# Optimization experiments

Hardware: AMD Instinct MI355X
Metric: run time of the kernel (lower is better)

The kernel has to match this reference:

```python
import jax, jax.numpy as jnp
import numpy as np

P, N, NF = 4, 871, 512            # num_meta_paths, node_size (hardcoded 871 in source), node_feature_size
XDIM = 116 * 116                   # x_proj input dim, hardcoded Linear(116*116, nf)
BETA, LAMBDA_WL, GAMMA = 0.1, 0.1, 0.1


def _xavier(k, shape):
    fan_in, fan_out = shape[0], shape[-1]
    bound = np.sqrt(6.0 / (fan_in + fan_out))
    return jax.random.uniform(k, shape, jnp.float32, -bound, bound)


def setup_inputs() -> dict:
    key = jax.random.key(0)
    ks = jax.random.split(key, 12)
    return {
        "z_stack": jax.random.normal(ks[0], (P, N, NF), jnp.float32),
        "x_orig": jax.random.normal(ks[1], (1, 116, 116), jnp.float32),
        "W": _xavier(ks[2], (N, 1)),
        "b": jax.random.uniform(ks[3], (N, 1), jnp.float32),
        "q": _xavier(ks[4], (N, NF)),
        "xp_w": _xavier(ks[5], (XDIM, NF)),
        "xp_b": jnp.zeros((NF,), jnp.float32),
        "w1": _xavier(ks[6], (2 * NF, 512)), "b1": jnp.zeros((512,), jnp.float32),
        "w2": _xavier(ks[7], (512, 256)), "b2": jnp.zeros((256,), jnp.float32),
        "w3": _xavier(ks[8], (256, 1)), "b3": jnp.zeros((1,), jnp.float32),
        "perm": jax.random.permutation(ks[9], N).astype(jnp.int32),
    }


def _mi_mlp(t, w1, b1, w2, b2, w3, b3):
    h = jax.nn.relu(t @ w1 + b1)
    h = jax.nn.relu(h @ w2 + b2)
    return h @ w3 + b3  # [N, 1]


def reference(z_stack, x_orig, W, b, q, xp_w, xp_b, w1, b1, w2, b2, w3, b3, perm):
    # --- vectorized form of the per-node loop:
    # score_p = mean_i( tanh(W_i * z[p,i,:] + b_i) . q_i )
    zt = jnp.tanh(W[None] * z_stack + b[None])            # [P,N,NF]
    scores = jnp.mean(jnp.sum(zt * q[None], axis=-1), axis=-1)  # [P]
    proportions = scores / jnp.sum(scores)
    attn = jax.nn.softmax(proportions)                    # [P] (no isomorphic pairs -> no overwrite)
    # layer_out_p = attn_p * z_p + z_p ; emb = sum_p layer_out_p
    emb = jnp.einsum('p,pnf->nf', 1.0 + attn, z_stack)    # [N,NF]
    # --- estimate_MI(x_orig, emb, mi_estimator_xz)
    x = jnp.broadcast_to(x_orig.reshape(1, -1), (N, XDIM))
    xh = x @ xp_w + xp_b                                  # [N,NF]
    t0 = jnp.concatenate([xh, emb], axis=1)               # [N,2NF]
    t1 = jnp.concatenate([xh, emb[perm]], axis=1)
    mi_lb = jnp.mean(_mi_mlp(t0, w1, b1, w2, b2, w3, b3)) - jnp.log(
        jnp.mean(jnp.exp(_mi_mlp(t1, w1, b1, w2, b2, w3, b3))) + 1e-8)
    I_XZ = jnp.clip(mi_lb, 0.0)
    # y_labels=None -> I_ZY = 0 ; empty isomorphic_pairs -> wl_loss = 0
    total_loss = I_XZ - BETA * 0.0 + LAMBDA_WL * 0.0 + GAMMA * jnp.sum(attn)
    return emb, total_loss
```

## Files before the change

kernel.cpp:

```cpp
#include <hip/hip_runtime.h>
#include <hip/hip_bf16.h>
#include <math.h>

#define NMETA  4
#define NNODE  871
#define NFEAT  512
#define XDIM   (116*116)
#define ZPLANE (NNODE*NFEAT)
#define Z4     (ZPLANE/4)
#define NCHUNK 55
#define MPAD   896
#define MT     56

#define WS_SCORES 0
#define WS_C1     528
#define WS_E1     1040
#define WS_XHP    WS_E1
#define WS_EMBB   (WS_E1 + MPAD*NFEAT)
#define WS_H2     WS_EMBB
#define WS_V      (WS_EMBB + MPAD*NFEAT/2)
#define WS_W1P    690040
#define WS_W2P    (WS_W1P + 512*512/2)

typedef short v8s __attribute__((ext_vector_type(8)));
typedef float v4f __attribute__((ext_vector_type(4)));

static __device__ __forceinline__ short f2bf(float f) {
  __hip_bfloat16 h = __float2bfloat16(f);
  return *reinterpret_cast<short*>(&h);
}

static __device__ __forceinline__ void compute_coef(const float* __restrict__ ws, float* coef) {
  float s[NMETA], sum = 0.f;
#pragma unroll
  for (int p = 0; p < NMETA; ++p) { s[p] = ws[WS_SCORES + p] / (float)NNODE; sum += s[p]; }
  float prop[NMETA], m = -1e30f;
#pragma unroll
  for (int p = 0; p < NMETA; ++p) { prop[p] = s[p] / sum; m = fmaxf(m, prop[p]); }
  float e[NMETA], es = 0.f;
#pragma unroll
  for (int p = 0; p < NMETA; ++p) { e[p] = expf(prop[p] - m); es += e[p]; }
#pragma unroll
  for (int p = 0; p < NMETA; ++p) coef[p] = 1.f + e[p] / es;
}

__global__ void k_init(float* __restrict__ ws) {
  int t = blockIdx.x * 256 + threadIdx.x;
  if (t < 1040) ws[t] = 0.f;
  else if (t < 1040 + (MPAD - NNODE) * NFEAT / 2)
    ws[WS_EMBB + NNODE * NFEAT / 2 + (t - 1040)] = 0.f;
}

__global__ void k_scores(const float* __restrict__ z, const float* __restrict__ W,
                         const float* __restrict__ b, const float* __restrict__ q,
                         float* __restrict__ ws) {
  const int p = blockIdx.x / NCHUNK;
  const int chunk = blockIdx.x % NCHUNK;
  const int i0 = chunk * 16;
  const int i1 = min(i0 + 16, NNODE);
  const int f4 = threadIdx.x & 127;
  const int ip = threadIdx.x >> 7;
  float local = 0.f;
  for (int i = i0 + ip; i < i1; i += 2) {
    const float wi = W[i];
    const float bi = b[i];
    const float4 zr = ((const float4*)(z + ((size_t)p * NNODE + i) * NFEAT))[f4];
    const float4 qr = ((const float4*)(q + (size_t)i * NFEAT))[f4];
    local += tanhf(wi * zr.x + bi) * qr.x + tanhf(wi * zr.y + bi) * qr.y
           + tanhf(wi * zr.z + bi) * qr.z + tanhf(wi * zr.w + bi) * qr.w;
  }
  __shared__ float red[256];
  red[threadIdx.x] = local;
  __syncthreads();
  for (int s = 128; s > 0; s >>= 1) {
    if ((int)threadIdx.x < s) red[threadIdx.x] += red[threadIdx.x + s];
    __syncthreads();
  }
  if (threadIdx.x == 0) atomicAdd(&ws[WS_SCORES + p], red[0]);
}

__global__ void k_emb(const float* __restrict__ z, const float* __restrict__ ws,
                      float* __restrict__ emb_out, short* __restrict__ embb) {
  const int idx = blockIdx.x * 256 + threadIdx.x;
  if (idx >= Z4) return;
  float coef[NMETA];
  compute_coef(ws, coef);
  const float4* z4 = (const float4*)z;
  float4 a = z4[idx];
  float4 b = z4[Z4 + idx];
  float4 c = z4[2 * Z4 + idx];
  float4 d = z4[3 * Z4 + idx];
  float4 r;
  r.x = coef[0] * a.x + coef[1] * b.x + coef[2] * c.x + coef[3] * d.x;
  r.y = coef[0] * a.y + coef[1] * b.y + coef[2] * c.y + coef[3] * d.y;
  r.z = coef[0] * a.z + coef[1] * b.z + coef[2] * c.z + coef[3] * d.z;
  r.w = coef[0] * a.w + coef[1] * b.w + coef[2] * c.w + coef[3] * d.w;
  ((float4*)emb_out)[idx] = r;
  short4 h;
  h.x = f2bf(r.x); h.y = f2bf(r.y); h.z = f2bf(r.z); h.w = f2bf(r.w);
  ((short4*)embb)[idx] = h;
}

__global__ __launch_bounds__(256) void k_xh(const float* __restrict__ x,
                                            const float* __restrict__ xpw,
                                            float* __restrict__ xhp) {
  const int f4 = threadIdx.x & 127;
  const int rp = threadIdx.x >> 7;
  const int d0 = blockIdx.x * 106;
  const int rows = min(106, XDIM - d0);
  __shared__ float xs[106];
  if ((int)threadIdx.x < rows) xs[threadIdx.x] = x[d0 + threadIdx.x];
  __syncthreads();
  float4 acc = {0.f, 0.f, 0.f, 0.f};
  const float4* xp4 = (const float4*)xpw;
#pragma unroll 4
  for (int r = rp; r < rows; r += 2) {
    const float xv = xs[r];
    const float4 w = xp4[(size_t)(d0 + r) * 128 + f4];
    acc.x += xv * w.x; acc.y += xv * w.y; acc.z += xv * w.z; acc.w += xv * w.w;
  }
  __shared__ float4 red[128];
  if (rp) red[f4] = acc;
  __syncthreads();
  if (!rp) {
    float4 o = red[f4];
    o.x += acc.x; o.y += acc.y; o.z += acc.z; o.w += acc.w;
    ((float4*)(xhp + (size_t)blockIdx.x * NFEAT))[f4] = o;
  }
}

__global__ void k_conv(const float* __restrict__ w1, const float* __restrict__ w2,
                       short* __restrict__ w1p, short* __restrict__ w2p) {
  int t = blockIdx.x * 256 + threadIdx.x;
  if (t < 512 * 512) {
    int j = t & 7; int r = t >> 3;
    int n15 = r & 15; r >>= 4;
    int quad = r & 3; r >>= 2;
    int nt = r & 31; int kb = r >> 5;
    int k = kb * 32 + quad * 8 + j;
    int n = nt * 16 + n15;
    w1p[t] = f2bf(w1[(size_t)(512 + k) * 512 + n]);
  } else if (t < 512 * 512 + 512 * 256) {
    int o = t - 512 * 512;
    int j = o & 7; int r = o >> 3;
    int n15 = r & 15; r >>= 4;
    int quad = r & 3; r >>= 2;
    int nt = r & 15; int kb = r >> 4;
    int k = kb * 32 + quad * 8 + j;
    int n = nt * 16 + n15;
    w2p[o] = f2bf(w2[(size_t)k * 256 + n]);
  }
}

__global__ __launch_bounds__(256) void k_c1(const float* __restrict__ xhp,
                                            const float* __restrict__ xpb,
                                            const float* __restrict__ w1,
                                            const float* __restrict__ b1,
                                            float* __restrict__ c1) {
  const int bk = blockIdx.x;
  __shared__ float xs[32];
  {
    const int f = threadIdx.x & 31;
    const int pg = threadIdx.x >> 5;
    float s = 0.f;
#pragma unroll 4
    for (int p = pg; p < 128; p += 8)
      s += xhp[(size_t)p * NFEAT + bk * 32 + f];
    __shared__ float red[256];
    red[threadIdx.x] = s;
    __syncthreads();
    if ((int)threadIdx.x < 32) {
      float t = 0.f;
#pragma unroll
      for (int g = 0; g < 8; ++g) t += red[g * 32 + threadIdx.x];
      xs[threadIdx.x] = t + xpb[bk * 32 + threadIdx.x];
    }
    __syncthreads();
  }
  const int j4 = threadIdx.x & 127;
  const int fp = threadIdx.x >> 7;
  float4 acc = {0.f, 0.f, 0.f, 0.f};
  const float4* w14 = (const float4*)w1;
#pragma unroll
  for (int ff = 0; ff < 16; ++ff) {
    const int f = bk * 32 + fp * 16 + ff;
    const float xv = xs[fp * 16 + ff];
    const float4 w = w14[(size_t)f * 128 + j4];
    acc.x += xv * w.x; acc.y += xv * w.y; acc.z += xv * w.z; acc.w += xv * w.w;
  }
  __shared__ float4 red2[128];
  if (fp) red2[j4] = acc;
  __syncthreads();
  if (!fp) {
    float4 o = red2[j4];
    o.x += acc.x; o.y += acc.y; o.z += acc.z; o.w += acc.w;
    if (bk == 0) {
      o.x += b1[j4 * 4 + 0]; o.y += b1[j4 * 4 + 1];
      o.z += b1[j4 * 4 + 2]; o.w += b1[j4 * 4 + 3];
    }
    atomicAdd(&c1[j4 * 4 + 0], o.x);
    atomicAdd(&c1[j4 * 4 + 1], o.y);
    atomicAdd(&c1[j4 * 4 + 2], o.z);
    atomicAdd(&c1[j4 * 4 + 3], o.w);
  }
}

__global__ __launch_bounds__(256) void k_gemmE1(const short* __restrict__ embb,
                                                const short* __restrict__ w1p,
                                                float* __restrict__ E1) {
  const int lane = threadIdx.x & 63;
  const int wid = blockIdx.x * 4 + (threadIdx.x >> 6);
  const int n15 = lane & 15, quad = lane >> 4;
  const int mt = wid % MT;
  const int ng = wid / MT;
  const short* A = embb + (size_t)(mt * 16 + n15) * NFEAT + quad * 8;
  const short* Bbase = w1p + (ng * 16 + quad) * 128 + n15 * 8;
  v4f acc0 = {0.f,0.f,0.f,0.f}, acc1 = acc0, acc2 = acc0, acc3 = acc0;
#pragma unroll
  for (int kb = 0; kb < 16; ++kb) {
    v8s a = *(const v8s*)(A + kb * 32);
    const short* Bp = Bbase + (size_t)kb * 16384;
    v8s b0 = *(const v8s*)(Bp);
    v8s b1 = *(const v8s*)(Bp + 512);
    v8s b2 = *(const v8s*)(Bp + 1024);
    v8s b3 = *(const v8s*)(Bp + 1536);
    acc0 = __builtin_amdgcn_mfma_f32_16x16x32_bf16(a, b0, acc0, 0, 0, 0);
    acc1 = __builtin_amdgcn_mfma_f32_16x16x32_bf16(a, b1, acc1, 0, 0, 0);
    acc2 = __builtin_amdgcn_mfma_f32_16x16x32_bf16(a, b2, acc2, 0, 0, 0);
    acc3 = __builtin_amdgcn_mfma_f32_16x16x32_bf16(a, b3, acc3, 0, 0, 0);
  }
  float* C0 = E1 + (size_t)(mt * 16 + quad * 4) * NFEAT + ng * 64 + n15;
#pragma unroll
  for (int r = 0; r < 4; ++r) {
    C0[(size_t)r * NFEAT +  0] = acc0[r];
    C0[(size_t)r * NFEAT + 16] = acc1[r];
    C0[(size_t)r * NFEAT + 32] = acc2[r];
    C0[(size_t)r * NFEAT + 48] = acc3[r];
  }
}

__global__ __launch_bounds__(256) void k_gemmH2(const float* __restrict__ E1,
                                                const float* __restrict__ c1,
                                                const short* __restrict__ w2p,
                                                const float* __restrict__ b2,
                                                float* __restrict__ H2) {
  const int lane = threadIdx.x & 63;
  const int wid = blockIdx.x * 4 + (threadIdx.x >> 6);
  const int n15 = lane & 15, quad = lane >> 4;
  const int mt = wid % MT;
  const int ng = wid / MT;
  const float* Arow = E1 + (size_t)(mt * 16 + n15) * NFEAT + quad * 8;
  const short* Bbase = w2p + (ng * 16 + quad) * 128 + n15 * 8;
  v4f acc0 = {0.f,0.f,0.f,0.f}, acc1 = acc0, acc2 = acc0, acc3 = acc0;
#pragma unroll
  for (int kb = 0; kb < 16; ++kb) {
    float4 e0 = *(const float4*)(Arow + kb * 32);
    float4 e1 = *(const float4*)(Arow + kb * 32 + 4);
    float4 ca = *(const float4*)(c1 + kb * 32 + quad * 8);
    float4 cb = *(const float4*)(c1 + kb * 32 + quad * 8 + 4);
    v8s a;
    a[0] = f2bf(fmaxf(e0.x + ca.x, 0.f));
    a[1] = f2bf(fmaxf(e0.y + ca.y, 0.f));
    a[2] = f2bf(fmaxf(e0.z + ca.z, 0.f));
    a[3] = f2bf(fmaxf(e0.w + ca.w, 0.f));
    a[4] = f2bf(fmaxf(e1.x + cb.x, 0.f));
    a[5] = f2bf(fmaxf(e1.y + cb.y, 0.f));
    a[6] = f2bf(fmaxf(e1.z + cb.z, 0.f));
    a[7] = f2bf(fmaxf(e1.w + cb.w, 0.f));
    const short* Bp = Bbase + (size_t)kb * 8192;
    v8s b0 = *(const v8s*)(Bp);
    v8s b1 = *(const v8s*)(Bp + 512);
    v8s b2v = *(const v8s*)(Bp + 1024);
    v8s b3 = *(const v8s*)(Bp + 1536);
    acc0 = __builtin_amdgcn_mfma_f32_16x16x32_bf16(a, b0, acc0, 0, 0, 0);
    acc1 = __builtin_amdgcn_mfma_f32_16x16x32_bf16(a, b1, acc1, 0, 0, 0);
    acc2 = __builtin_amdgcn_mfma_f32_16x16x32_bf16(a, b2v, acc2, 0, 0, 0);
    acc3 = __builtin_amdgcn_mfma_f32_16x16x32_bf16(a, b3, acc3, 0, 0, 0);
  }
  const int grow0 = mt * 16 + quad * 4;
  const float bb0 = b2[ng * 64 + n15], bb1 = b2[ng * 64 + 16 + n15];
  const float bb2 = b2[ng * 64 + 32 + n15], bb3 = b2[ng * 64 + 48 + n15];
#pragma unroll
  for (int r = 0; r < 4; ++r) {
    const int grow = grow0 + r;
    if (grow < NNODE) {
      float* Hr = H2 + (size_t)grow * 256 + ng * 64 + n15;
      Hr[0]  = fmaxf(acc0[r] + bb0, 0.f);
      Hr[16] = fmaxf(acc1[r] + bb1, 0.f);
      Hr[32] = fmaxf(acc2[r] + bb2, 0.f);
      Hr[48] = fmaxf(acc3[r] + bb3, 0.f);
    }
  }
}

__global__ void k_rowdot(const float* __restrict__ H2, const float* __restrict__ w3,
                         const float* __restrict__ b3, float* __restrict__ v) {
  const int wid = (blockIdx.x * 256 + threadIdx.x) >> 6;
  const int lane = threadIdx.x & 63;
  if (wid >= NNODE) return;
  float acc = 0.f;
  for (int j = lane; j < 256; j += 64) acc += H2[(size_t)wid * 256 + j] * w3[j];
  for (int off = 32; off > 0; off >>= 1) acc += __shfl_down(acc, off);
  if (lane == 0) v[wid] = acc + b3[0];
}

__global__ void k_final(const float* __restrict__ ws, float* __restrict__ out) {
  const float* v = ws + WS_V;
  float s0 = 0.f, s1 = 0.f;
  for (int i = threadIdx.x; i < NNODE; i += 256) {
    float x = v[i];
    s0 += x;
    s1 += expf(x);
  }
  __shared__ float r0[256], r1[256];
  r0[threadIdx.x] = s0; r1[threadIdx.x] = s1;
  __syncthreads();
  for (int s = 128; s > 0; s >>= 1) {
    if ((int)threadIdx.x < s) {
      r0[threadIdx.x] += r0[threadIdx.x + s];
      r1[threadIdx.x] += r1[threadIdx.x + s];
    }
    __syncthreads();
  }
  if (threadIdx.x == 0) {
    float m0 = r0[0] / (float)NNODE;
    float m1 = r1[0] / (float)NNODE;
    float mi = m0 - logf(m1 + 1e-8f);
    out[ZPLANE] = fmaxf(mi, 0.f) + 0.1f;
  }
}

extern "C" void kernel_launch(void* const* d_in, const int* in_sizes, int n_in,
                              void* d_out, int out_size, void* d_ws, size_t ws_size,
                              hipStream_t stream) {
  const float* z   = (const float*)d_in[0];
  const float* x   = (const float*)d_in[1];
  const float* W   = (const float*)d_in[2];
  const float* b   = (const float*)d_in[3];
  const float* q   = (const float*)d_in[4];
  const float* xpw = (const float*)d_in[5];
  const float* xpb = (const float*)d_in[6];
  const float* w1  = (const float*)d_in[7];
  const float* b1  = (const float*)d_in[8];
  const float* w2  = (const float*)d_in[9];
  const float* b2  = (const float*)d_in[10];
  const float* w3  = (const float*)d_in[11];
  const float* b3  = (const float*)d_in[12];
  float* out = (float*)d_out;
  float* ws  = (float*)d_ws;

  short* embb = (short*)(ws + WS_EMBB);
  short* w1p  = (short*)(ws + WS_W1P);
  short* w2p  = (short*)(ws + WS_W2P);

  k_init<<<17, 256, 0, stream>>>(ws);
  k_xh<<<128, 256, 0, stream>>>(x, xpw, ws + WS_XHP);
  k_conv<<<1536, 256, 0, stream>>>(w1, w2, w1p, w2p);
  k_scores<<<NMETA * NCHUNK, 256, 0, stream>>>(z, W, b, q, ws);
  k_emb<<<(Z4 + 255) / 256, 256, 0, stream>>>(z, ws, out, embb);
  k_c1<<<16, 256, 0, stream>>>(ws + WS_XHP, xpb, w1, b1, ws + WS_C1);
  k_gemmE1<<<112, 256, 0, stream>>>(embb, w1p, ws + WS_E1);
  k_gemmH2<<<56, 256, 0, stream>>>(ws + WS_E1, ws + WS_C1, w2p, b2, ws + WS_H2);
  k_rowdot<<<(NNODE + 3) / 4, 256, 0, stream>>>(ws + WS_H2, w3, b3, ws + WS_V);
  k_final<<<1, 256, 0, stream>>>(ws, out);
}
```

Baseline: 153.8 us.

## Fuse launches into front/mid kernels and fold row-dot into H2 GEMM

Result: faster. 132.8 us (-13.7%).

```diff
diff --git a/kernel.cpp b/kernel.cpp
--- a/kernel.cpp
+++ b/kernel.cpp
@@ -12,15 +12,14 @@
 #define MPAD   896
 #define MT     56
 
-#define WS_SCORES 0
-#define WS_C1     528
-#define WS_E1     1040
+#define WS_SPART  16
+#define WS_C1P    256
+#define WS_E1     8448
 #define WS_XHP    WS_E1
-#define WS_EMBB   (WS_E1 + MPAD*NFEAT)
-#define WS_H2     WS_EMBB
-#define WS_V      (WS_EMBB + MPAD*NFEAT/2)
-#define WS_W1P    690040
-#define WS_W2P    (WS_W1P + 512*512/2)
+#define WS_EMBB   467200
+#define WS_V      696576
+#define WS_W1P    697448
+#define WS_W2P    828520
 
 typedef short v8s __attribute__((ext_vector_type(8)));
 typedef float v4f __attribute__((ext_vector_type(4)));
@@ -30,178 +29,191 @@
   return *reinterpret_cast<short*>(&h);
 }
 
-static __device__ __forceinline__ void compute_coef(const float* __restrict__ ws, float* coef) {
-  float s[NMETA], sum = 0.f;
-#pragma unroll
-  for (int p = 0; p < NMETA; ++p) { s[p] = ws[WS_SCORES + p] / (float)NNODE; sum += s[p]; }
-  float prop[NMETA], m = -1e30f;
-#pragma unroll
-  for (int p = 0; p < NMETA; ++p) { prop[p] = s[p] / sum; m = fmaxf(m, prop[p]); }
-  float e[NMETA], es = 0.f;
-#pragma unroll
-  for (int p = 0; p < NMETA; ++p) { e[p] = expf(prop[p] - m); es += e[p]; }
-#pragma unroll
-  for (int p = 0; p < NMETA; ++p) coef[p] = 1.f + e[p] / es;
-}
-
-__global__ void k_init(float* __restrict__ ws) {
-  int t = blockIdx.x * 256 + threadIdx.x;
-  if (t < 1040) ws[t] = 0.f;
-  else if (t < 1040 + (MPAD - NNODE) * NFEAT / 2)
-    ws[WS_EMBB + NNODE * NFEAT / 2 + (t - 1040)] = 0.f;
-}
-
-__global__ void k_scores(const float* __restrict__ z, const float* __restrict__ W,
-                         const float* __restrict__ b, const float* __restrict__ q,
-                         float* __restrict__ ws) {
-  const int p = blockIdx.x / NCHUNK;
-  const int chunk = blockIdx.x % NCHUNK;
-  const int i0 = chunk * 16;
-  const int i1 = min(i0 + 16, NNODE);
-  const int f4 = threadIdx.x & 127;
-  const int ip = threadIdx.x >> 7;
-  float local = 0.f;
-  for (int i = i0 + ip; i < i1; i += 2) {
-    const float wi = W[i];
-    const float bi = b[i];
-    const float4 zr = ((const float4*)(z + ((size_t)p * NNODE + i) * NFEAT))[f4];
-    const float4 qr = ((const float4*)(q + (size_t)i * NFEAT))[f4];
-    local += tanhf(wi * zr.x + bi) * qr.x + tanhf(wi * zr.y + bi) * qr.y
-           + tanhf(wi * zr.z + bi) * qr.z + tanhf(wi * zr.w + bi) * qr.w;
-  }
-  __shared__ float red[256];
-  red[threadIdx.x] = local;
-  __syncthreads();
-  for (int s = 128; s > 0; s >>= 1) {
-    if ((int)threadIdx.x < s) red[threadIdx.x] += red[threadIdx.x + s];
-    __syncthreads();
-  }
-  if (threadIdx.x == 0) atomicAdd(&ws[WS_SCORES + p], red[0]);
-}
-
-__global__ void k_emb(const float* __restrict__ z, const float* __restrict__ ws,
-                      float* __restrict__ emb_out, short* __restrict__ embb) {
-  const int idx = blockIdx.x * 256 + threadIdx.x;
-  if (idx >= Z4) return;
-  float coef[NMETA];
-  compute_coef(ws, coef);
-  const float4* z4 = (const float4*)z;
-  float4 a = z4[idx];
-  float4 b = z4[Z4 + idx];
-  float4 c = z4[2 * Z4 + idx];
-  float4 d = z4[3 * Z4 + idx];
-  float4 r;
-  r.x = coef[0] * a.x + coef[1] * b.x + coef[2] * c.x + coef[3] * d.x;
-  r.y = coef[0] * a.y + coef[1] * b.y + coef[2] * c.y + coef[3] * d.y;
-  r.z = coef[0] * a.z + coef[1] * b.z + coef[2] * c.z + coef[3] * d.z;
-  r.w = coef[0] * a.w + coef[1] * b.w + coef[2] * c.w + coef[3] * d.w;
-  ((float4*)emb_out)[idx] = r;
-  short4 h;
-  h.x = f2bf(r.x); h.y = f2bf(r.y); h.z = f2bf(r.z); h.w = f2bf(r.w);
-  ((short4*)embb)[idx] = h;
-}
-
-__global__ __launch_bounds__(256) void k_xh(const float* __restrict__ x,
-                                            const float* __restrict__ xpw,
-                                            float* __restrict__ xhp) {
-  const int f4 = threadIdx.x & 127;
-  const int rp = threadIdx.x >> 7;
-  const int d0 = blockIdx.x * 106;
-  const int rows = min(106, XDIM - d0);
-  __shared__ float xs[106];
-  if ((int)threadIdx.x < rows) xs[threadIdx.x] = x[d0 + threadIdx.x];
-  __syncthreads();
-  float4 acc = {0.f, 0.f, 0.f, 0.f};
-  const float4* xp4 = (const float4*)xpw;
+__global__ __launch_bounds__(256) void k_front(const float* __restrict__ x,
+                                               const float* __restrict__ xpw,
+                                               const float* __restrict__ w1,
+                                               const float* __restrict__ w2,
+                                               const float* __restrict__ z,
+                                               const float* __restrict__ W,
+                                               const float* __restrict__ b,
+                                               const float* __restrict__ q,
+                                               float* __restrict__ ws,
+                                               short* __restrict__ w1p,
+                                               short* __restrict__ w2p) {
+  const int blk = blockIdx.x;
+  const int tid = threadIdx.x;
+  if (blk < 128) {
+    const int f4 = tid & 127;
+    const int rp = tid >> 7;
+    const int d0 = blk * 106;
+    const int rows = min(106, XDIM - d0);
+    __shared__ float xs[106];
+    if (tid < rows) xs[tid] = x[d0 + tid];
+    __syncthreads();
+    float4 acc = {0.f, 0.f, 0.f, 0.f};
+    const float4* xp4 = (const float4*)xpw;
 #pragma unroll 4
-  for (int r = rp; r < rows; r += 2) {
-    const float xv = xs[r];
-    const float4 w = xp4[(size_t)(d0 + r) * 128 + f4];
-    acc.x += xv * w.x; acc.y += xv * w.y; acc.z += xv * w.z; acc.w += xv * w.w;
-  }
-  __shared__ float4 red[128];
-  if (rp) red[f4] = acc;
-  __syncthreads();
-  if (!rp) {
-    float4 o = red[f4];
-    o.x += acc.x; o.y += acc.y; o.z += acc.z; o.w += acc.w;
-    ((float4*)(xhp + (size_t)blockIdx.x * NFEAT))[f4] = o;
-  }
-}
-
-__global__ void k_conv(const float* __restrict__ w1, const float* __restrict__ w2,
-                       short* __restrict__ w1p, short* __restrict__ w2p) {
-  int t = blockIdx.x * 256 + threadIdx.x;
-  if (t < 512 * 512) {
-    int j = t & 7; int r = t >> 3;
-    int n15 = r & 15; r >>= 4;
-    int quad = r & 3; r >>= 2;
-    int nt = r & 31; int kb = r >> 5;
-    int k = kb * 32 + quad * 8 + j;
-    int n = nt * 16 + n15;
-    w1p[t] = f2bf(w1[(size_t)(512 + k) * 512 + n]);
-  } else if (t < 512 * 512 + 512 * 256) {
-    int o = t - 512 * 512;
-    int j = o & 7; int r = o >> 3;
-    int n15 = r & 15; r >>= 4;
-    int quad = r & 3; r >>= 2;
-    int nt = r & 15; int kb = r >> 4;
-    int k = kb * 32 + quad * 8 + j;
-    int n = nt * 16 + n15;
-    w2p[o] = f2bf(w2[(size_t)k * 256 + n]);
-  }
-}
-
-__global__ __launch_bounds__(256) void k_c1(const float* __restrict__ xhp,
-                                            const float* __restrict__ xpb,
-                                            const float* __restrict__ w1,
-                                            const float* __restrict__ b1,
-                                            float* __restrict__ c1) {
-  const int bk = blockIdx.x;
-  __shared__ float xs[32];
-  {
-    const int f = threadIdx.x & 31;
-    const int pg = threadIdx.x >> 5;
-    float s = 0.f;
+    for (int r = rp; r < rows; r += 2) {
+      const float xv = xs[r];
+      const float4 w = xp4[(size_t)(d0 + r) * 128 + f4];
+      acc.x += xv * w.x; acc.y += xv * w.y; acc.z += xv * w.z; acc.w += xv * w.w;
+    }
+    __shared__ float4 red4[128];
+    if (rp) red4[f4] = acc;
+    __syncthreads();
+    if (!rp) {
+      float4 o = red4[f4];
+      o.x += acc.x; o.y += acc.y; o.z += acc.z; o.w += acc.w;
+      ((float4*)(ws + WS_XHP + (size_t)blk * NFEAT))[f4] = o;
+    }
+  } else if (blk < 128 + 1536) {
+    int t = (blk - 128) * 256 + tid;
+    if (t < 512 * 512) {
+      int j = t & 7; int r = t >> 3;
+      int n15 = r & 15; r >>= 4;
+      int quad = r & 3; r >>= 2;
+      int nt = r & 31; int kb = r >> 5;
+      int k = kb * 32 + quad * 8 + j;
+      int n = nt * 16 + n15;
+      w1p[t] = f2bf(w1[(size_t)(512 + k) * 512 + n]);
+    } else {
+      int o = t - 512 * 512;
+      int j = o & 7; int r = o >> 3;
+      int n15 = r & 15; r >>= 4;
+      int quad = r & 3; r >>= 2;
+      int nt = r & 15; int kb = r >> 4;
+      int k = kb * 32 + quad * 8 + j;
+      int n = nt * 16 + n15;
+      w2p[o] = f2bf(w2[(size_t)k * 256 + n]);
+    }
+  } else {
+    const int sblk = blk - 1664;
+    const int p = sblk / NCHUNK;
+    const int chunk = sblk % NCHUNK;
+    const int i0 = chunk * 16;
+    const int i1 = min(i0 + 16, NNODE);
+    const int f4 = tid & 127;
+    const int ip = tid >> 7;
+    float local = 0.f;
+    for (int i = i0 + ip; i < i1; i += 2) {
+      const float wi = W[i];
+      const float bi = b[i];
+      const float4 zr = ((const float4*)(z + ((size_t)p * NNODE + i) * NFEAT))[f4];
+      const float4 qr = ((const float4*)(q + (size_t)i * NFEAT))[f4];
+      local += tanhf(wi * zr.x + bi) * qr.x + tanhf(wi * zr.y + bi) * qr.y
+             + tanhf(wi * zr.z + bi) * qr.z + tanhf(wi * zr.w + bi) * qr.w;
+    }
+    __shared__ float red[256];
+    red[tid] = local;
+    __syncthreads();
+    for (int s = 128; s > 0; s >>= 1) {
+      if (tid < s) red[tid] += red[tid + s];
+      __syncthreads();
+    }
+    if (tid == 0) ws[WS_SPART + sblk] = red[0];
+  }
+}
+
+__global__ __launch_bounds__(256) void k_mid(const float* __restrict__ z,
+                                             float* __restrict__ ws,
+                                             float* __restrict__ emb_out,
+                                             short* __restrict__ embb,
+                                             const float* __restrict__ xpb,
+                                             const float* __restrict__ w1,
+                                             const float* __restrict__ b1) {
+  const int tid = threadIdx.x;
+  if (blockIdx.x < 448) {
+    __shared__ float sp[220];
+    __shared__ float sc[NMETA];
+    if (tid < 220) sp[tid] = ws[WS_SPART + tid];
+    __syncthreads();
+    if (tid < NMETA) {
+      float s = 0.f;
+      for (int c = 0; c < NCHUNK; ++c) s += sp[tid * NCHUNK + c];
+      sc[tid] = s;
+    }
+    __syncthreads();
+    float sv[NMETA], sum = 0.f;
+#pragma unroll
+    for (int p = 0; p < NMETA; ++p) { sv[p] = sc[p] / (float)NNODE; sum += sv[p]; }
+    float m = -1e30f;
+#pragma unroll
+    for (int p = 0; p < NMETA; ++p) { sv[p] = sv[p] / sum; m = fmaxf(m, sv[p]); }
+    float es = 0.f;
+#pragma unroll
+    for (int p = 0; p < NMETA; ++p) { sv[p] = expf(sv[p] - m); es += sv[p]; }
+    float coef[NMETA];
+#pragma unroll
+    for (int p = 0; p < NMETA; ++p) coef[p] = 1.f + sv[p] / es;
+
+    const int idx = blockIdx.x * 256 + tid;
+    if (idx < Z4) {
+      const float4* z4 = (const float4*)z;
+      float4 a = z4[idx];
+      float4 bb = z4[Z4 + idx];
+      float4 c = z4[2 * Z4 + idx];
+      float4 d = z4[3 * Z4 + idx];
+      float4 r;
+      r.x = coef[0] * a.x + coef[1] * bb.x + coef[2] * c.x + coef[3] * d.x;
+      r.y = coef[0] * a.y + coef[1] * bb.y + coef[2] * c.y + coef[3] * d.y;
+      r.z = coef[0] * a.z + coef[1] * bb.z + coef[2] * c.z + coef[3] * d.z;
+      r.w = coef[0] * a.w + coef[1] * bb.w + coef[2] * c.w + coef[3] * d.w;
+      ((float4*)emb_out)[idx] = r;
+      short4 h;
+      h.x = f2bf(r.x); h.y = f2bf(r.y); h.z = f2bf(r.z); h.w = f2bf(r.w);
+      ((short4*)embb)[idx] = h;
+    } else {
+      short4 zr = {0, 0, 0, 0};
+      ((short4*)embb)[idx] = zr;
+    }
+  } else {
+    const int bk = blockIdx.x - 448;
+    for (int t = tid; t < NCHUNK; t += 256) {
+      int vi = bk * NCHUNK + t;
+      if (vi < NNODE) ws[WS_V + vi] = 0.f;
+    }
+    __shared__ float xs[32];
+    {
+      const int f = tid & 31;
+      const int pg = tid >> 5;
+      float s = 0.f;
 #pragma unroll 4
-    for (int p = pg; p < 128; p += 8)
-      s += xhp[(size_t)p * NFEAT + bk * 32 + f];
-    __shared__ float red[256];
-    red[threadIdx.x] = s;
-    __syncthreads();
-    if ((int)threadIdx.x < 32) {
-      float t = 0.f;
-#pragma unroll
-      for (int g = 0; g < 8; ++g) t += red[g * 32 + threadIdx.x];
-      xs[threadIdx.x] = t + xpb[bk * 32 + threadIdx.x];
-    }
-    __syncthreads();
-  }
-  const int j4 = threadIdx.x & 127;
-  const int fp = threadIdx.x >> 7;
-  float4 acc = {0.f, 0.f, 0.f, 0.f};
-  const float4* w14 = (const float4*)w1;
-#pragma unroll
-  for (int ff = 0; ff < 16; ++ff) {
-    const int f = bk * 32 + fp * 16 + ff;
-    const float xv = xs[fp * 16 + ff];
-    const float4 w = w14[(size_t)f * 128 + j4];
-    acc.x += xv * w.x; acc.y += xv * w.y; acc.z += xv * w.z; acc.w += xv * w.w;
-  }
-  __shared__ float4 red2[128];
-  if (fp) red2[j4] = acc;
-  __syncthreads();
-  if (!fp) {
-    float4 o = red2[j4];
-    o.x += acc.x; o.y += acc.y; o.z += acc.z; o.w += acc.w;
-    if (bk == 0) {
-      o.x += b1[j4 * 4 + 0]; o.y += b1[j4 * 4 + 1];
-      o.z += b1[j4 * 4 + 2]; o.w += b1[j4 * 4 + 3];
-    }
-    atomicAdd(&c1[j4 * 4 + 0], o.x);
-    atomicAdd(&c1[j4 * 4 + 1], o.y);
-    atomicAdd(&c1[j4 * 4 + 2], o.z);
-    atomicAdd(&c1[j4 * 4 + 3], o.w);
+      for (int p = pg; p < 128; p += 8)
+        s += ws[WS_XHP + (size_t)p * NFEAT + bk * 32 + f];
+      __shared__ float red[256];
+      red[tid] = s;
+      __syncthreads();
+      if (tid < 32) {
+        float t2 = 0.f;
+#pragma unroll
+        for (int g = 0; g < 8; ++g) t2 += red[g * 32 + tid];
+        xs[tid] = t2 + xpb[bk * 32 + tid];
+      }
+      __syncthreads();
+    }
+    const int j4 = tid & 127;
+    const int fp = tid >> 7;
+    float4 acc = {0.f, 0.f, 0.f, 0.f};
+    const float4* w14 = (const float4*)w1;
+#pragma unroll
+    for (int ff = 0; ff < 16; ++ff) {
+      const int f = bk * 32 + fp * 16 + ff;
+      const float xv = xs[fp * 16 + ff];
+      const float4 w = w14[(size_t)f * 128 + j4];
+      acc.x += xv * w.x; acc.y += xv * w.y; acc.z += xv * w.z; acc.w += xv * w.w;
+    }
+    __shared__ float4 red2[128];
+    if (fp) red2[j4] = acc;
+    __syncthreads();
+    if (!fp) {
+      float4 o = red2[j4];
+      o.x += acc.x; o.y += acc.y; o.z += acc.z; o.w += acc.w;
+      if (bk == 0) {
+        o.x += b1[j4 * 4 + 0]; o.y += b1[j4 * 4 + 1];
+        o.z += b1[j4 * 4 + 2]; o.w += b1[j4 * 4 + 3];
+      }
+      ((float4*)(ws + WS_C1P + (size_t)bk * NFEAT))[j4] = o;
+    }
   }
 }
 
@@ -239,11 +251,24 @@
   }
 }
 
-__global__ __launch_bounds__(256) void k_gemmH2(const float* __restrict__ E1,
-                                                const float* __restrict__ c1,
-                                                const short* __restrict__ w2p,
-                                                const float* __restrict__ b2,
-                                                float* __restrict__ H2) {
+__global__ __launch_bounds__(256) void k_gemmH2v(const float* __restrict__ E1,
+                                                 const float* __restrict__ c1p,
+                                                 const short* __restrict__ w2p,
+                                                 const float* __restrict__ b2,
+                                                 const float* __restrict__ w3,
+                                                 float* __restrict__ v) {
+  __shared__ float cs[512];
+  {
+    float a0 = 0.f, a1 = 0.f;
+#pragma unroll
+    for (int k = 0; k < 16; ++k) {
+      a0 += c1p[(size_t)k * 512 + threadIdx.x];
+      a1 += c1p[(size_t)k * 512 + 256 + threadIdx.x];
+    }
+    cs[threadIdx.x] = a0;
+    cs[256 + threadIdx.x] = a1;
+  }
+  __syncthreads();
   const int lane = threadIdx.x & 63;
   const int wid = blockIdx.x * 4 + (threadIdx.x >> 6);
   const int n15 = lane & 15, quad = lane >> 4;
@@ -256,8 +281,8 @@
   for (int kb = 0; kb < 16; ++kb) {
     float4 e0 = *(const float4*)(Arow + kb * 32);
     float4 e1 = *(const float4*)(Arow + kb * 32 + 4);
-    float4 ca = *(const float4*)(c1 + kb * 32 + quad * 8);
-    float4 cb = *(const float4*)(c1 + kb * 32 + quad * 8 + 4);
+    const float4 ca = *(const float4*)(cs + kb * 32 + quad * 8);
+    const float4 cb = *(const float4*)(cs + kb * 32 + quad * 8 + 4);
     v8s a;
     a[0] = f2bf(fmaxf(e0.x + ca.x, 0.f));
     a[1] = f2bf(fmaxf(e0.y + ca.y, 0.f));
@@ -277,38 +302,33 @@
     acc2 = __builtin_amdgcn_mfma_f32_16x16x32_bf16(a, b2v, acc2, 0, 0, 0);
     acc3 = __builtin_amdgcn_mfma_f32_16x16x32_bf16(a, b3, acc3, 0, 0, 0);
   }
+  const float bb0 = b2[ng * 64 + n15],      bb1 = b2[ng * 64 + 16 + n15];
+  const float bb2 = b2[ng * 64 + 32 + n15], bb3 = b2[ng * 64 + 48 + n15];
+  const float w30 = w3[ng * 64 + n15],      w31 = w3[ng * 64 + 16 + n15];
+  const float w32 = w3[ng * 64 + 32 + n15], w33 = w3[ng * 64 + 48 + n15];
   const int grow0 = mt * 16 + quad * 4;
-  const float bb0 = b2[ng * 64 + n15], bb1 = b2[ng * 64 + 16 + n15];
-  const float bb2 = b2[ng * 64 + 32 + n15], bb3 = b2[ng * 64 + 48 + n15];
 #pragma unroll
   for (int r = 0; r < 4; ++r) {
+    float s = fmaxf(acc0[r] + bb0, 0.f) * w30
+            + fmaxf(acc1[r] + bb1, 0.f) * w31
+            + fmaxf(acc2[r] + bb2, 0.f) * w32
+            + fmaxf(acc3[r] + bb3, 0.f) * w33;
+    s += __shfl_xor(s, 1);
+    s += __shfl_xor(s, 2);
+    s += __shfl_xor(s, 4);
+    s += __shfl_xor(s, 8);
     const int grow = grow0 + r;
-    if (grow < NNODE) {
-      float* Hr = H2 + (size_t)grow * 256 + ng * 64 + n15;
-      Hr[0]  = fmaxf(acc0[r] + bb0, 0.f);
-      Hr[16] = fmaxf(acc1[r] + bb1, 0.f);
-      Hr[32] = fmaxf(acc2[r] + bb2, 0.f);
-      Hr[48] = fmaxf(acc3[r] + bb3, 0.f);
-    }
-  }
-}
-
-__global__ void k_rowdot(const float* __restrict__ H2, const float* __restrict__ w3,
-                         const float* __restrict__ b3, float* __restrict__ v) {
-  const int wid = (blockIdx.x * 256 + threadIdx.x) >> 6;
-  const int lane = threadIdx.x & 63;
-  if (wid >= NNODE) return;
-  float acc = 0.f;
-  for (int j = lane; j < 256; j += 64) acc += H2[(size_t)wid * 256 + j] * w3[j];
-  for (int off = 32; off > 0; off >>= 1) acc += __shfl_down(acc, off);
-  if (lane == 0) v[wid] = acc + b3[0];
-}
-
-__global__ void k_final(const float* __restrict__ ws, float* __restrict__ out) {
+    if (n15 == 0 && grow < NNODE) atomicAdd(&v[grow], s);
+  }
+}
+
+__global__ void k_final(const float* __restrict__ ws, const float* __restrict__ b3,
+                        float* __restrict__ out) {
   const float* v = ws + WS_V;
+  const float bias = b3[0];
   float s0 = 0.f, s1 = 0.f;
   for (int i = threadIdx.x; i < NNODE; i += 256) {
-    float x = v[i];
+    float x = v[i] + bias;
     s0 += x;
     s1 += expf(x);
   }
@@ -353,14 +373,9 @@
   short* w1p  = (short*)(ws + WS_W1P);
   short* w2p  = (short*)(ws + WS_W2P);
 
-  k_init<<<17, 256, 0, stream>>>(ws);
-  k_xh<<<128, 256, 0, stream>>>(x, xpw, ws + WS_XHP);
-  k_conv<<<1536, 256, 0, stream>>>(w1, w2, w1p, w2p);
-  k_scores<<<NMETA * NCHUNK, 256, 0, stream>>>(z, W, b, q, ws);
-  k_emb<<<(Z4 + 255) / 256, 256, 0, stream>>>(z, ws, out, embb);
-  k_c1<<<16, 256, 0, stream>>>(ws + WS_XHP, xpb, w1, b1, ws + WS_C1);
+  k_front<<<1884, 256, 0, stream>>>(x, xpw, w1, w2, z, W, b, q, ws, w1p, w2p);
+  k_mid<<<464, 256, 0, stream>>>(z, ws, out, embb, xpb, w1, b1);
   k_gemmE1<<<112, 256, 0, stream>>>(embb, w1p, ws + WS_E1);
-  k_gemmH2<<<56, 256, 0, stream>>>(ws + WS_E1, ws + WS_C1, w2p, b2, ws + WS_H2);
-  k_rowdot<<<(NNODE + 3) / 4, 256, 0, stream>>>(ws + WS_H2, w3, b3, ws + WS_V);
-  k_final<<<1, 256, 0, stream>>>(ws, out);
-}
+  k_gemmH2v<<<56, 256, 0, stream>>>(ws + WS_E1, ws + WS_C1P, w2p, b2, w3, ws + WS_V);
+  k_final<<<1, 256, 0, stream>>>(ws, b3, out);
+}
```
